# Kernel tuning notes

Measured on AMD Instinct MI355X. Metric: run time of the kernel, lower is better.

Reference implementation:

```python
import jax, jax.numpy as jnp
import numpy as np

H, C = 2, 32  # heads, out_channels per head
NEG_SLOPE = 0.2


def gatv2_layer(h, src, dst, ea, W, b, We, att, bias, N):
    # shared lin_l = lin_r (share_weights=True)
    z = (h @ W + b).reshape(N, H, C)                      # [N,H,C]
    e = (ea @ We).reshape(-1, H, C)                        # [E',H,C]
    s = jax.nn.leaky_relu(z[dst] + z[src] + e, NEG_SLOPE)  # [E',H,C]
    alpha = jnp.einsum('ehc,hc->eh', s, att)               # [E',H]
    # segment softmax over destination neighborhoods
    m = jax.ops.segment_max(alpha, dst, num_segments=N)
    m = jnp.where(jnp.isfinite(m), m, 0.0)
    ex = jnp.exp(alpha - m[dst])
    denom = jax.ops.segment_sum(ex, dst, num_segments=N)
    a = ex / (denom[dst] + 1e-16)                          # [E',H]
    msg = (z[src] * a[:, :, None]).reshape(-1, H * C)      # [E',H*C]
    out = jax.ops.segment_sum(msg, dst, num_segments=N) + bias
    return out                                             # [N,H*C]


def setup_inputs() -> dict:
    key = jax.random.key(0)
    ks = jax.random.split(key, 16)
    N, E = 50000, 800000
    inp = {
        'x': jax.random.normal(ks[0], (N, 2), jnp.float32),
        'edge_index': jax.random.randint(ks[1], (2, E), 0, N, jnp.int64 if jax.config.jax_enable_x64 else jnp.int32).astype(jnp.int32),
        'edge_attr': jax.random.uniform(ks[2], (E, 2), jnp.float32),
        'dest_index': 123,
        'W0': jax.random.normal(ks[3], (2, 64), jnp.float32) * 0.5,
        'b0': jnp.zeros((64,), jnp.float32),
        'We0': jax.random.normal(ks[4], (2, 64), jnp.float32) * 0.5,
        'att0': jax.random.normal(ks[5], (H, C), jnp.float32) * 0.5,
        'bias0': jnp.zeros((64,), jnp.float32),
        'W1': jax.random.normal(ks[6], (64, 64), jnp.float32) * 0.125,
        'b1': jnp.zeros((64,), jnp.float32),
        'We1': jax.random.normal(ks[7], (2, 64), jnp.float32) * 0.5,
        'att1': jax.random.normal(ks[8], (H, C), jnp.float32) * 0.5,
        'bias1': jnp.zeros((64,), jnp.float32),
        'Wm1': jax.random.normal(ks[9], (194, 32), jnp.float32) * 0.07,
        'bm1': jnp.zeros((32,), jnp.float32),
        'Wm2': jax.random.normal(ks[10], (32, 1), jnp.float32) * 0.17,
        'bm2': jnp.zeros((1,), jnp.float32),
    }
    return inp


def reference(x, edge_index, edge_attr, dest_index,
              W0, b0, We0, att0, bias0,
              W1, b1, We1, att1, bias1,
              Wm1, bm1, Wm2, bm2):
    N = x.shape[0]
    # add self loops (fill_value='mean' for edge_attr)
    loops = jnp.arange(N, dtype=edge_index.dtype)
    src = jnp.concatenate([edge_index[0], loops])
    dst = jnp.concatenate([edge_index[1], loops])
    ea_sl = jnp.concatenate(
        [edge_attr, jnp.broadcast_to(edge_attr.mean(axis=0), (N, edge_attr.shape[1]))], axis=0)

    h = x
    h = jax.nn.elu(gatv2_layer(h, src, dst, ea_sl, W0, b0, We0, att0, bias0, N))
    h = jax.nn.elu(gatv2_layer(h, src, dst, ea_sl, W1, b1, We1, att1, bias1, N))

    goal = h[dest_index]                                   # [64]
    src_emb = h[edge_index[0]]                             # [E,64]
    dst_emb = h[edge_index[1]]                             # [E,64]
    goal_rep = jnp.broadcast_to(goal, (edge_index.shape[1], goal.shape[0]))
    edge_in = jnp.concatenate([src_emb, dst_emb, goal_rep, edge_attr], axis=-1)  # [E,194]
    hmlp = jax.nn.relu(edge_in @ Wm1 + bm1)
    logits = (hmlp @ Wm2 + bm2).squeeze(-1)                # [E]
    return logits
```

## Files before the change

### kernel.cpp

```cpp
#include <hip/hip_runtime.h>
#include <hip/hip_bf16.h>
#include <math.h>


typedef __attribute__((ext_vector_type(8))) short short8;
typedef __attribute__((ext_vector_type(4))) float f32x4;

#define BSH 7
#define CH 4096

template <int IMM>
__device__ __forceinline__ float swz(float x) {
    return __int_as_float(__builtin_amdgcn_ds_swizzle(__float_as_int(x), IMM));
}

template <int CTRL>
__device__ __forceinline__ float dpp_add(float p) {
    int t = __builtin_amdgcn_update_dpp(0, __float_as_int(p), CTRL, 0xF, 0xF, true);
    return p + __int_as_float(t);
}

__device__ __forceinline__ float head_reduce(float p) {
    p = dpp_add<0xB1>(p);
    p = dpp_add<0x4E>(p);
    p = dpp_add<0x141>(p);
    p = dpp_add<0x140>(p);
    p += swz<0x401F>(p);
    return p;
}

__device__ __forceinline__ short2 bsplit(float x) {
    unsigned u = __float_as_uint(x);
    short hi = (short)(u >> 16);
    float hif = __uint_as_float(u & 0xFFFF0000u);
    short lo = (short)(__float_as_uint(x - hif) >> 16);
    return make_short2(hi, lo);
}

__global__ void init_kernel(int* __restrict__ bucket_base, float* __restrict__ easum,
                            int nbuck) {
    int i = blockIdx.x * blockDim.x + threadIdx.x;
    if (i < nbuck) bucket_base[i] = 0;
    if (i < 2) easum[i] = 0.f;
}

__global__ __launch_bounds__(256) void easum_kernel(const float2* __restrict__ ea,
                                                    float* __restrict__ easum, int E) {
    __shared__ float r0[4], r1[4];
    int stride = gridDim.x * blockDim.x;
    float s0 = 0.f, s1 = 0.f;
    for (int e = blockIdx.x * blockDim.x + threadIdx.x; e < E; e += stride) {
        float2 v = ea[e];
        s0 += v.x; s1 += v.y;
    }
#pragma unroll
    for (int o = 32; o >= 1; o >>= 1) {
        s0 += __shfl_xor(s0, o);
        s1 += __shfl_xor(s1, o);
    }
    int wave = threadIdx.x >> 6;
    if ((threadIdx.x & 63) == 0) { r0[wave] = s0; r1[wave] = s1; }
    __syncthreads();
    if (threadIdx.x == 0) {
        atomicAdd(&easum[0], r0[0] + r0[1] + r0[2] + r0[3]);
        atomicAdd(&easum[1], r1[0] + r1[1] + r1[2] + r1[3]);
    }
}

__global__ __launch_bounds__(256) void bhist_kernel(const int* __restrict__ ei,
                                                    int* __restrict__ bucket_base,
                                                    int E, int EP, int nbuck) {
    extern __shared__ int lcnt[];
    int tid = threadIdx.x;
    for (int i = tid; i < nbuck; i += 256) lcnt[i] = 0;
    __syncthreads();
    int base = blockIdx.x * CH;
    int end = min(base + CH, EP);
    for (int i = base + tid; i < end; i += 256) {
        int d = (i < E) ? ei[E + i] : (i - E);
        atomicAdd(&lcnt[d >> BSH], 1);
    }
    __syncthreads();
    for (int i = tid; i < nbuck; i += 256) {
        int c = lcnt[i];
        if (c) atomicAdd(&bucket_base[i], c);
    }
}

__global__ __launch_bounds__(256) void bscan_kernel(int* __restrict__ bucket_base,
                                                    int* __restrict__ bucket_cursor,
                                                    int* __restrict__ row_ptr,
                                                    int N, int nbuck) {
    __shared__ int sm[256];
    int tid = threadIdx.x;
    int K = (nbuck + 255) / 256;
    int b0 = tid * K;
    int local = 0;
    for (int k = 0; k < K; ++k) {
        int b = b0 + k;
        if (b < nbuck) local += bucket_base[b];
    }
    sm[tid] = local;
    __syncthreads();
    for (int st = 1; st < 256; st <<= 1) {
        int v = sm[tid];
        int a = (tid >= st) ? sm[tid - st] : 0;
        __syncthreads();
        sm[tid] = v + a;
        __syncthreads();
    }
    int run = (tid == 0) ? 0 : sm[tid - 1];
    for (int k = 0; k < K; ++k) {
        int b = b0 + k;
        if (b < nbuck) {
            int c = bucket_base[b];
            bucket_base[b] = run;
            bucket_cursor[b] = run;
            run += c;
        }
    }
    if (tid == 255) {
        bucket_base[nbuck] = sm[255];
        row_ptr[N] = sm[255];
    }
}

__global__ __launch_bounds__(256) void phaseA_kernel(const int* __restrict__ ei,
                                                     const float2* __restrict__ ea,
                                                     const float* __restrict__ easum,
                                                     int* __restrict__ bucket_cursor,
                                                     float4* __restrict__ staged,
                                                     int E, int EP, int nbuck) {
    extern __shared__ int sm[];
    int* lcnt = sm;
    int* lbase = sm + nbuck;
    int tid = threadIdx.x;
    for (int i = tid; i < nbuck; i += 256) lcnt[i] = 0;
    __syncthreads();
    int base = blockIdx.x * CH;
    int end = min(base + CH, EP);
    for (int i = base + tid; i < end; i += 256) {
        int d = (i < E) ? ei[E + i] : (i - E);
        atomicAdd(&lcnt[d >> BSH], 1);
    }
    __syncthreads();
    for (int i = tid; i < nbuck; i += 256) {
        int c = lcnt[i];
        lbase[i] = c ? atomicAdd(&bucket_cursor[i], c) : 0;
        lcnt[i] = 0;
    }
    __syncthreads();
    float inv = 1.f / (float)E;
    float m0 = easum[0] * inv, m1 = easum[1] * inv;
    for (int i = base + tid; i < end; i += 256) {
        int s, d; float ex, ey;
        if (i < E) {
            s = ei[i]; d = ei[E + i];
            float2 v = ea[i]; ex = v.x; ey = v.y;
        } else {
            s = d = i - E; ex = m0; ey = m1;
        }
        int b = d >> BSH;
        int pos = lbase[b] + atomicAdd(&lcnt[b], 1);
        staged[pos] = make_float4(__int_as_float(s), ex, ey, __int_as_float(d));
    }
}

__global__ __launch_bounds__(256) void phaseB_kernel(const float4* __restrict__ staged,
                                                     const int* __restrict__ bucket_base,
                                                     int* __restrict__ row_ptr,
                                                     float4* __restrict__ recs, int N) {
    __shared__ int cnt128[128];
    __shared__ int offs[128];
    int b = blockIdx.x;
    int n0 = b << BSH;
    int tid = threadIdx.x;
    if (tid < 128) cnt128[tid] = 0;
    __syncthreads();
    int begs = bucket_base[b];
    int ends = bucket_base[b + 1];
    for (int i = begs + tid; i < ends; i += 256) {
        int d = __float_as_int(staged[i].w);
        atomicAdd(&cnt128[d - n0], 1);
    }
    __syncthreads();
    if (tid < 128) offs[tid] = cnt128[tid];
    __syncthreads();
    for (int st = 1; st < 128; st <<= 1) {
        int v = 0;
        if (tid < 128) {
            v = offs[tid];
            if (tid >= st) v += offs[tid - st];
        }
        __syncthreads();
        if (tid < 128) offs[tid] = v;
        __syncthreads();
    }
    if (tid < 128) {
        int excl = begs + offs[tid] - cnt128[tid];
        int node = n0 + tid;
        if (node < N) row_ptr[node] = excl;
        offs[tid] = excl;
    }
    __syncthreads();
    for (int i = begs + tid; i < ends; i += 256) {
        float4 r = staged[i];
        int d = __float_as_int(r.w);
        int pos = atomicAdd(&offs[d - n0], 1);
        recs[pos] = r;
    }
}

__global__ __launch_bounds__(512) void bfrag_kernel(const float* __restrict__ W1,
                                                    const float* __restrict__ Wm1,
                                                    short* __restrict__ BfW1,
                                                    short* __restrict__ BfWm) {
    int snt = threadIdx.x >> 6;
    int lane = threadIdx.x & 63;
    int s = snt >> 2, nt = snt & 3;
    int col = nt * 16 + (lane & 15);
    short* Bf = blockIdx.x == 0 ? BfW1 : BfWm;
#pragma unroll
    for (int j = 0; j < 8; ++j) {
        int k = s * 32 + (lane >> 4) * 8 + j;
        float v;
        if (blockIdx.x == 0) {
            v = W1[k * 64 + col];
        } else {
            v = (col < 32) ? Wm1[k * 32 + col] : Wm1[(64 + k) * 32 + (col - 32)];
        }
        short2 t = bsplit(v);
        Bf[(snt * 2 + 0) * 512 + lane * 8 + j] = t.x;
        Bf[(snt * 2 + 1) * 512 + lane * 8 + j] = t.y;
    }
}

__global__ __launch_bounds__(256) void mfma_gemm64(const float* __restrict__ h,
                                                   const short* __restrict__ Bf,
                                                   const float* __restrict__ bias,
                                                   float* __restrict__ out, int N) {
    int wave = threadIdx.x >> 6;
    int lane = threadIdx.x & 63;
    int n0 = blockIdx.x * 64 + wave * 16;
    if (n0 >= N) return;
    int m = lane & 15, quad = lane >> 4;
    int arow = n0 + m;
    if (arow > N - 1) arow = N - 1;

    f32x4 acc[4] = {{0.f, 0.f, 0.f, 0.f}, {0.f, 0.f, 0.f, 0.f},
                    {0.f, 0.f, 0.f, 0.f}, {0.f, 0.f, 0.f, 0.f}};
#pragma unroll
    for (int s = 0; s < 2; ++s) {
        const float* ap = h + (size_t)arow * 64 + s * 32 + quad * 8;
        float4 a0 = *(const float4*)ap;
        float4 a1 = *(const float4*)(ap + 4);
        short8 ahi, alo;
        short2 t;
        t = bsplit(a0.x); ahi[0] = t.x; alo[0] = t.y;
        t = bsplit(a0.y); ahi[1] = t.x; alo[1] = t.y;
        t = bsplit(a0.z); ahi[2] = t.x; alo[2] = t.y;
        t = bsplit(a0.w); ahi[3] = t.x; alo[3] = t.y;
        t = bsplit(a1.x); ahi[4] = t.x; alo[4] = t.y;
        t = bsplit(a1.y); ahi[5] = t.x; alo[5] = t.y;
        t = bsplit(a1.z); ahi[6] = t.x; alo[6] = t.y;
        t = bsplit(a1.w); ahi[7] = t.x; alo[7] = t.y;
#pragma unroll
        for (int nt = 0; nt < 4; ++nt) {
            const short* bp = Bf + ((s * 4 + nt) * 2) * 512 + lane * 8;
            short8 bhi = *(const short8*)bp;
            short8 blo = *(const short8*)(bp + 512);
            acc[nt] = __builtin_amdgcn_mfma_f32_16x16x32_bf16(ahi, bhi, acc[nt], 0, 0, 0);
            acc[nt] = __builtin_amdgcn_mfma_f32_16x16x32_bf16(ahi, blo, acc[nt], 0, 0, 0);
            acc[nt] = __builtin_amdgcn_mfma_f32_16x16x32_bf16(alo, bhi, acc[nt], 0, 0, 0);
        }
    }
#pragma unroll
    for (int nt = 0; nt < 4; ++nt) {
        int col = nt * 16 + m;
        float bj = bias ? bias[col] : 0.f;
#pragma unroll
        for (int r = 0; r < 4; ++r) {
            int orow = n0 + quad * 4 + r;
            if (orow < N) out[(size_t)orow * 64 + col] = acc[nt][r] + bj;
        }
    }
}

__global__ __launch_bounds__(256) void agg0_kernel(
    const float2* __restrict__ x, const float* __restrict__ W0,
    const float* __restrict__ b0, const int* __restrict__ row_ptr,
    const float4* __restrict__ recs,
    const float* __restrict__ We, const float* __restrict__ att,
    const float* __restrict__ bias, float* __restrict__ hout, int N) {
    int gtid = blockIdx.x * blockDim.x + threadIdx.x;
    int n = gtid >> 6;
    if (n >= N) return;
    n = __builtin_amdgcn_readfirstlane(n);
    int lane = threadIdx.x & 63;

    float W0a = W0[lane], W0b = W0[64 + lane], b0c = b0[lane];
    float We0 = We[lane], We1 = We[64 + lane];
    float attj = att[lane];
    float2 xn = x[n];
    float zn = fmaf(xn.x, W0a, fmaf(xn.y, W0b, b0c));

    int beg = row_ptr[n], end = row_ptr[n + 1];
    float ll[4] = {0.f, 0.f, 0.f, 0.f};
    float aa[4] = {0.f, 0.f, 0.f, 0.f};
    int i = beg;
    for (; i + 7 < end; i += 8) {
        float w[8], zsv[8];
#pragma unroll
        for (int k = 0; k < 8; ++k) {
            float4 r = recs[i + k];
            int s = __builtin_amdgcn_readfirstlane(__float_as_int(r.x));
            float2 xs = x[s];
            float zs = fmaf(xs.x, W0a, fmaf(xs.y, W0b, b0c));
            float sj = zn + zs + fmaf(r.y, We0, r.z * We1);
            sj = fmaxf(sj, 0.2f * sj);
            float alpha = head_reduce(sj * attj);
            w[k] = __expf(fminf(alpha, 60.f));
            zsv[k] = zs;
        }
#pragma unroll
        for (int k = 0; k < 8; ++k) {
            ll[k & 3] += w[k];
            aa[k & 3] = fmaf(w[k], zsv[k], aa[k & 3]);
        }
    }
    for (; i < end; ++i) {
        float4 r = recs[i];
        int s = __builtin_amdgcn_readfirstlane(__float_as_int(r.x));
        float2 xs = x[s];
        float zs = fmaf(xs.x, W0a, fmaf(xs.y, W0b, b0c));
        float sj = zn + zs + fmaf(r.y, We0, r.z * We1);
        sj = fmaxf(sj, 0.2f * sj);
        float alpha = head_reduce(sj * attj);
        float w = __expf(fminf(alpha, 60.f));
        ll[0] += w;
        aa[0] = fmaf(w, zs, aa[0]);
    }
    float l = (ll[0] + ll[1]) + (ll[2] + ll[3]);
    float acc = (aa[0] + aa[1]) + (aa[2] + aa[3]);
    float v = acc / (l + 1e-16f) + bias[lane];
    v = (v > 0.f) ? v : expm1f(v);
    hout[n * 64 + lane] = v;
}

__global__ __launch_bounds__(256) void agg1_kernel(
    const float* __restrict__ z, const int* __restrict__ row_ptr,
    const float4* __restrict__ recs,
    const float* __restrict__ We, const float* __restrict__ att,
    const float* __restrict__ bias, float* __restrict__ hout, int N) {
    int gtid = blockIdx.x * blockDim.x + threadIdx.x;
    int n = gtid >> 6;
    if (n >= N) return;
    n = __builtin_amdgcn_readfirstlane(n);
    int lane = threadIdx.x & 63;

    float We0 = We[lane], We1 = We[64 + lane];
    float attj = att[lane];
    float zn = z[n * 64 + lane];

    int beg = row_ptr[n], end = row_ptr[n + 1];
    float ll[4] = {0.f, 0.f, 0.f, 0.f};
    float aa[4] = {0.f, 0.f, 0.f, 0.f};
    int i = beg;
    for (; i + 7 < end; i += 8) {
        float w[8], zsv[8];
#pragma unroll
        for (int k = 0; k < 8; ++k) {
            float4 r = recs[i + k];
            int s = __builtin_amdgcn_readfirstlane(__float_as_int(r.x));
            float zs = z[s * 64 + lane];
            float sj = zn + zs + fmaf(r.y, We0, r.z * We1);
            sj = fmaxf(sj, 0.2f * sj);
            float alpha = head_reduce(sj * attj);
            w[k] = __expf(fminf(alpha, 60.f));
            zsv[k] = zs;
        }
#pragma unroll
        for (int k = 0; k < 8; ++k) {
            ll[k & 3] += w[k];
            aa[k & 3] = fmaf(w[k], zsv[k], aa[k & 3]);
        }
    }
    for (; i < end; ++i) {
        float4 r = recs[i];
        int s = __builtin_amdgcn_readfirstlane(__float_as_int(r.x));
        float zs = z[s * 64 + lane];
        float sj = zn + zs + fmaf(r.y, We0, r.z * We1);
        sj = fmaxf(sj, 0.2f * sj);
        float alpha = head_reduce(sj * attj);
        float w = __expf(fminf(alpha, 60.f));
        ll[0] += w;
        aa[0] = fmaf(w, zs, aa[0]);
    }
    float l = (ll[0] + ll[1]) + (ll[2] + ll[3]);
    float acc = (aa[0] + aa[1]) + (aa[2] + aa[3]);
    float v = acc / (l + 1e-16f) + bias[lane];
    v = (v > 0.f) ? v : expm1f(v);
    hout[n * 64 + lane] = v;
}

__global__ void gvec_kernel(const float* __restrict__ h, const float* __restrict__ Wm1,
                            const float* __restrict__ bm1, const int* __restrict__ dest,
                            float* __restrict__ gvec) {
    int q = threadIdx.x;
    if (q >= 32) return;
    int d = dest[0];
    float acc = bm1[q];
    for (int k = 0; k < 64; ++k)
        acc = fmaf(h[d * 64 + k], Wm1[(128 + k) * 32 + q], acc);
    gvec[q] = acc;
}

__global__ __launch_bounds__(256) void edge_mlp_kernel(
    const int* __restrict__ ei, const float2* __restrict__ ea,
    const float* __restrict__ hsd, const float* __restrict__ gvec,
    const float* __restrict__ WrowA, const float* __restrict__ WrowB,
    const float* __restrict__ Wm2, const float* __restrict__ bm2,
    float* __restrict__ out, int E) {
    int tid = blockIdx.x * blockDim.x + threadIdx.x;
    int e = tid >> 3;
    int j = tid & 7;
    if (e >= E) return;
    int s = ei[e], d = ei[E + e];
    float2 eav = ea[e];
    float4 a = *(const float4*)(hsd + (size_t)s * 64 + j * 4);
    float4 bv = *(const float4*)(hsd + (size_t)d * 64 + 32 + j * 4);
    float4 g = *(const float4*)(gvec + j * 4);
    float4 wa = *(const float4*)(WrowA + j * 4);
    float4 wb = *(const float4*)(WrowB + j * 4);
    float4 w2 = *(const float4*)(Wm2 + j * 4);
    float acc = 0.f, v;
    v = fmaf(eav.x, wa.x, fmaf(eav.y, wb.x, a.x + bv.x + g.x)); v = fmaxf(v, 0.f); acc = fmaf(v, w2.x, acc);
    v = fmaf(eav.x, wa.y, fmaf(eav.y, wb.y, a.y + bv.y + g.y)); v = fmaxf(v, 0.f); acc = fmaf(v, w2.y, acc);
    v = fmaf(eav.x, wa.z, fmaf(eav.y, wb.z, a.z + bv.z + g.z)); v = fmaxf(v, 0.f); acc = fmaf(v, w2.z, acc);
    v = fmaf(eav.x, wa.w, fmaf(eav.y, wb.w, a.w + bv.w + g.w)); v = fmaxf(v, 0.f); acc = fmaf(v, w2.w, acc);
    acc = dpp_add<0xB1>(acc);
    acc = dpp_add<0x4E>(acc);
    acc = dpp_add<0x141>(acc);
    if (j == 0) out[e] = acc + bm2[0];
}

extern "C" void kernel_launch(void* const* d_in, const int* in_sizes, int n_in,
                              void* d_out, int out_size, void* d_ws, size_t ws_size,
                              hipStream_t stream) {
    const float* x     = (const float*)d_in[0];
    const int*   ei    = (const int*)d_in[1];
    const float* ea    = (const float*)d_in[2];
    const int*   dest  = (const int*)d_in[3];
    const float* W0    = (const float*)d_in[4];
    const float* b0    = (const float*)d_in[5];
    const float* We0   = (const float*)d_in[6];
    const float* att0  = (const float*)d_in[7];
    const float* bias0 = (const float*)d_in[8];
    const float* W1    = (const float*)d_in[9];
    const float* b1    = (const float*)d_in[10];
    const float* We1   = (const float*)d_in[11];
    const float* att1  = (const float*)d_in[12];
    const float* bias1 = (const float*)d_in[13];
    const float* Wm1   = (const float*)d_in[14];
    const float* bm1   = (const float*)d_in[15];
    const float* Wm2   = (const float*)d_in[16];
    const float* bm2   = (const float*)d_in[17];

    const int N = in_sizes[0] / 2;
    const int E = in_sizes[1] / 2;
    const int EP = E + N;
    const int nbuck = (N + 127) >> BSH;
    const int nchunk = (EP + CH - 1) / CH;

    char* ws = (char*)d_ws;
    size_t off = 0;
    auto alloc = [&](size_t bytes) -> void* {
        void* p = ws + off;
        off += bytes;
        off = (off + 255) & ~(size_t)255;
        return p;
    };
    int*    bucket_base   = (int*)alloc((size_t)(nbuck + 1) * 4);
    int*    bucket_cursor = (int*)alloc((size_t)nbuck * 4);
    int*    row_ptr       = (int*)alloc((size_t)(N + 1) * 4);
    size_t  shared_bytes  = (size_t)EP * 16 > (size_t)N * 256 ? (size_t)EP * 16
                                                              : (size_t)N * 256;
    float4* staged        = (float4*)alloc(shared_bytes);
    float4* recs          = (float4*)alloc((size_t)EP * 16);
    float*  hbuf          = (float*)alloc((size_t)N * 64 * 4);
    float*  easum         = (float*)alloc(8);
    float*  gvec          = (float*)alloc(32 * 4);
    short*  BfW1          = (short*)alloc(8192 * 2);
    short*  BfWm          = (short*)alloc(8192 * 2);
    float*  zbuf          = (float*)staged;
    float*  hsd           = zbuf;

    dim3 blk(256);
    init_kernel<<<(nbuck + 255) / 256, blk, 0, stream>>>(bucket_base, easum, nbuck);
    easum_kernel<<<128, blk, 0, stream>>>((const float2*)ea, easum, E);
    bhist_kernel<<<nchunk, blk, (size_t)nbuck * 4, stream>>>(ei, bucket_base, E, EP, nbuck);
    bscan_kernel<<<1, blk, 0, stream>>>(bucket_base, bucket_cursor, row_ptr, N, nbuck);
    phaseA_kernel<<<nchunk, blk, (size_t)nbuck * 8, stream>>>(ei, (const float2*)ea, easum,
                                                              bucket_cursor, staged, E, EP, nbuck);
    phaseB_kernel<<<nbuck, blk, 0, stream>>>(staged, bucket_base, row_ptr, recs, N);
    bfrag_kernel<<<2, 512, 0, stream>>>(W1, Wm1, BfW1, BfWm);
    agg0_kernel<<<(N * 64 + 255) / 256, blk, 0, stream>>>((const float2*)x, W0, b0,
                                                          row_ptr, recs,
                                                          We0, att0, bias0, hbuf, N);
    mfma_gemm64<<<(N + 63) / 64, blk, 0, stream>>>(hbuf, BfW1, b1, zbuf, N);
    agg1_kernel<<<(N * 64 + 255) / 256, blk, 0, stream>>>(zbuf, row_ptr, recs,
                                                          We1, att1, bias1, hbuf, N);
    gvec_kernel<<<1, 64, 0, stream>>>(hbuf, Wm1, bm1, dest, gvec);
    mfma_gemm64<<<(N + 63) / 64, blk, 0, stream>>>(hbuf, BfWm, (const float*)nullptr, hsd, N);
    edge_mlp_kernel<<<((size_t)E * 8 + 255) / 256, blk, 0, stream>>>(
        ei, (const float2*)ea, hsd, gvec,
        Wm1 + 192 * 32, Wm1 + 193 * 32, Wm2, bm2, (float*)d_out, E);
}
```

Measured before the change: 293.0 us.

## Fuse setup kernels and batch attention head reductions across eight edges

Merges the init, easum, histogram, bfrag and gvec launches into fewer kernels (setup_kernel, pre_kernel, and gvec folded into the second GEMM), which removes several tiny launches. In both aggregation kernels the per-edge full head reduction is replaced by a partial DPP reduction per edge. Eight edges' partials are then interleaved across lanes so a single final reduce and a single exp serve all eight, and the results are broadcast back with swizzles. The scalar tail loop is removed by clamping record indices and masking weights. This cuts cross-lane and transcendental work per edge, at the cost of extra selects and some wasted work on padded tail iterations.

```diff
diff --git a/kernel.cpp b/kernel.cpp
--- a/kernel.cpp
+++ b/kernel.cpp
@@ -18,15 +18,6 @@
 __device__ __forceinline__ float dpp_add(float p) {
     int t = __builtin_amdgcn_update_dpp(0, __float_as_int(p), CTRL, 0xF, 0xF, true);
     return p + __int_as_float(t);
-}
-
-__device__ __forceinline__ float head_reduce(float p) {
-    p = dpp_add<0xB1>(p);
-    p = dpp_add<0x4E>(p);
-    p = dpp_add<0x141>(p);
-    p = dpp_add<0x140>(p);
-    p += swz<0x401F>(p);
-    return p;
 }
 
 __device__ __forceinline__ short2 bsplit(float x) {
@@ -37,19 +28,49 @@
     return make_short2(hi, lo);
 }
 
-__global__ void init_kernel(int* __restrict__ bucket_base, float* __restrict__ easum,
-                            int nbuck) {
-    int i = blockIdx.x * blockDim.x + threadIdx.x;
-    if (i < nbuck) bucket_base[i] = 0;
-    if (i < 2) easum[i] = 0.f;
-}
-
-__global__ __launch_bounds__(256) void easum_kernel(const float2* __restrict__ ea,
-                                                    float* __restrict__ easum, int E) {
+__global__ __launch_bounds__(512) void setup_kernel(const float* __restrict__ W1,
+                                                    const float* __restrict__ Wm1,
+                                                    short* __restrict__ BfW1,
+                                                    short* __restrict__ BfWm,
+                                                    int* __restrict__ bucket_base,
+                                                    float* __restrict__ easum, int nbuck) {
+    if (blockIdx.x == 2) {
+        for (int i = threadIdx.x; i <= nbuck; i += 512) bucket_base[i] = 0;
+        if (threadIdx.x < 2) easum[threadIdx.x] = 0.f;
+        return;
+    }
+    int snt = threadIdx.x >> 6;
+    int lane = threadIdx.x & 63;
+    int s = snt >> 2, nt = snt & 3;
+    int col = nt * 16 + (lane & 15);
+    short* Bf = blockIdx.x == 0 ? BfW1 : BfWm;
+#pragma unroll
+    for (int j = 0; j < 8; ++j) {
+        int k = s * 32 + (lane >> 4) * 8 + j;
+        float v;
+        if (blockIdx.x == 0) {
+            v = W1[k * 64 + col];
+        } else {
+            v = (col < 32) ? Wm1[k * 32 + col] : Wm1[(64 + k) * 32 + (col - 32)];
+        }
+        short2 t = bsplit(v);
+        Bf[(snt * 2 + 0) * 512 + lane * 8 + j] = t.x;
+        Bf[(snt * 2 + 1) * 512 + lane * 8 + j] = t.y;
+    }
+}
+
+__global__ __launch_bounds__(256) void pre_kernel(const int* __restrict__ ei,
+                                                  const float2* __restrict__ ea,
+                                                  int* __restrict__ bucket_base,
+                                                  float* __restrict__ easum,
+                                                  int E, int EP, int nbuck) {
+    extern __shared__ int lcnt[];
     __shared__ float r0[4], r1[4];
-    int stride = gridDim.x * blockDim.x;
+    int tid = threadIdx.x;
+    for (int i = tid; i < nbuck; i += 256) lcnt[i] = 0;
     float s0 = 0.f, s1 = 0.f;
-    for (int e = blockIdx.x * blockDim.x + threadIdx.x; e < E; e += stride) {
+    int estride = gridDim.x * 256;
+    for (int e = blockIdx.x * 256 + tid; e < E; e += estride) {
         float2 v = ea[e];
         s0 += v.x; s1 += v.y;
     }
@@ -58,21 +79,8 @@
         s0 += __shfl_xor(s0, o);
         s1 += __shfl_xor(s1, o);
     }
-    int wave = threadIdx.x >> 6;
-    if ((threadIdx.x & 63) == 0) { r0[wave] = s0; r1[wave] = s1; }
-    __syncthreads();
-    if (threadIdx.x == 0) {
-        atomicAdd(&easum[0], r0[0] + r0[1] + r0[2] + r0[3]);
-        atomicAdd(&easum[1], r1[0] + r1[1] + r1[2] + r1[3]);
-    }
-}
-
-__global__ __launch_bounds__(256) void bhist_kernel(const int* __restrict__ ei,
-                                                    int* __restrict__ bucket_base,
-                                                    int E, int EP, int nbuck) {
-    extern __shared__ int lcnt[];
-    int tid = threadIdx.x;
-    for (int i = tid; i < nbuck; i += 256) lcnt[i] = 0;
+    int wave = tid >> 6;
+    if ((tid & 63) == 0) { r0[wave] = s0; r1[wave] = s1; }
     __syncthreads();
     int base = blockIdx.x * CH;
     int end = min(base + CH, EP);
@@ -81,6 +89,10 @@
         atomicAdd(&lcnt[d >> BSH], 1);
     }
     __syncthreads();
+    if (tid == 0) {
+        atomicAdd(&easum[0], r0[0] + r0[1] + r0[2] + r0[3]);
+        atomicAdd(&easum[1], r1[0] + r1[1] + r1[2] + r1[3]);
+    }
     for (int i = tid; i < nbuck; i += 256) {
         int c = lcnt[i];
         if (c) atomicAdd(&bucket_base[i], c);
@@ -211,81 +223,6 @@
     }
 }
 
-__global__ __launch_bounds__(512) void bfrag_kernel(const float* __restrict__ W1,
-                                                    const float* __restrict__ Wm1,
-                                                    short* __restrict__ BfW1,
-                                                    short* __restrict__ BfWm) {
-    int snt = threadIdx.x >> 6;
-    int lane = threadIdx.x & 63;
-    int s = snt >> 2, nt = snt & 3;
-    int col = nt * 16 + (lane & 15);
-    short* Bf = blockIdx.x == 0 ? BfW1 : BfWm;
-#pragma unroll
-    for (int j = 0; j < 8; ++j) {
-        int k = s * 32 + (lane >> 4) * 8 + j;
-        float v;
-        if (blockIdx.x == 0) {
-            v = W1[k * 64 + col];
-        } else {
-            v = (col < 32) ? Wm1[k * 32 + col] : Wm1[(64 + k) * 32 + (col - 32)];
-        }
-        short2 t = bsplit(v);
-        Bf[(snt * 2 + 0) * 512 + lane * 8 + j] = t.x;
-        Bf[(snt * 2 + 1) * 512 + lane * 8 + j] = t.y;
-    }
-}
-
-__global__ __launch_bounds__(256) void mfma_gemm64(const float* __restrict__ h,
-                                                   const short* __restrict__ Bf,
-                                                   const float* __restrict__ bias,
-                                                   float* __restrict__ out, int N) {
-    int wave = threadIdx.x >> 6;
-    int lane = threadIdx.x & 63;
-    int n0 = blockIdx.x * 64 + wave * 16;
-    if (n0 >= N) return;
-    int m = lane & 15, quad = lane >> 4;
-    int arow = n0 + m;
-    if (arow > N - 1) arow = N - 1;
-
-    f32x4 acc[4] = {{0.f, 0.f, 0.f, 0.f}, {0.f, 0.f, 0.f, 0.f},
-                    {0.f, 0.f, 0.f, 0.f}, {0.f, 0.f, 0.f, 0.f}};
-#pragma unroll
-    for (int s = 0; s < 2; ++s) {
-        const float* ap = h + (size_t)arow * 64 + s * 32 + quad * 8;
-        float4 a0 = *(const float4*)ap;
-        float4 a1 = *(const float4*)(ap + 4);
-        short8 ahi, alo;
-        short2 t;
-        t = bsplit(a0.x); ahi[0] = t.x; alo[0] = t.y;
-        t = bsplit(a0.y); ahi[1] = t.x; alo[1] = t.y;
-        t = bsplit(a0.z); ahi[2] = t.x; alo[2] = t.y;
-        t = bsplit(a0.w); ahi[3] = t.x; alo[3] = t.y;
-        t = bsplit(a1.x); ahi[4] = t.x; alo[4] = t.y;
-        t = bsplit(a1.y); ahi[5] = t.x; alo[5] = t.y;
-        t = bsplit(a1.z); ahi[6] = t.x; alo[6] = t.y;
-        t = bsplit(a1.w); ahi[7] = t.x; alo[7] = t.y;
-#pragma unroll
-        for (int nt = 0; nt < 4; ++nt) {
-            const short* bp = Bf + ((s * 4 + nt) * 2) * 512 + lane * 8;
-            short8 bhi = *(const short8*)bp;
-            short8 blo = *(const short8*)(bp + 512);
-            acc[nt] = __builtin_amdgcn_mfma_f32_16x16x32_bf16(ahi, bhi, acc[nt], 0, 0, 0);
-            acc[nt] = __builtin_amdgcn_mfma_f32_16x16x32_bf16(ahi, blo, acc[nt], 0, 0, 0);
-            acc[nt] = __builtin_amdgcn_mfma_f32_16x16x32_bf16(alo, bhi, acc[nt], 0, 0, 0);
-        }
-    }
-#pragma unroll
-    for (int nt = 0; nt < 4; ++nt) {
-        int col = nt * 16 + m;
-        float bj = bias ? bias[col] : 0.f;
-#pragma unroll
-        for (int r = 0; r < 4; ++r) {
-            int orow = n0 + quad * 4 + r;
-            if (orow < N) out[(size_t)orow * 64 + col] = acc[nt][r] + bj;
-        }
-    }
-}
-
 __global__ __launch_bounds__(256) void agg0_kernel(
     const float2* __restrict__ x, const float* __restrict__ W0,
     const float* __restrict__ b0, const int* __restrict__ row_ptr,
@@ -297,6 +234,7 @@
     if (n >= N) return;
     n = __builtin_amdgcn_readfirstlane(n);
     int lane = threadIdx.x & 63;
+    bool c0 = lane & 1, c1 = lane & 2, c2 = lane & 4;
 
     float W0a = W0[lane], W0b = W0[64 + lane], b0c = b0[lane];
     float We0 = We[lane], We1 = We[64 + lane];
@@ -307,44 +245,54 @@
     int beg = row_ptr[n], end = row_ptr[n + 1];
     float ll[4] = {0.f, 0.f, 0.f, 0.f};
     float aa[4] = {0.f, 0.f, 0.f, 0.f};
-    int i = beg;
-    for (; i + 7 < end; i += 8) {
-        float w[8], zsv[8];
+    for (int i = beg; i < end; i += 8) {
+        float p[8], zs[8], ry[8], rz[8];
 #pragma unroll
         for (int k = 0; k < 8; ++k) {
-            float4 r = recs[i + k];
+            int idx = i + k; if (idx > end - 1) idx = end - 1;
+            float4 r = recs[idx];
             int s = __builtin_amdgcn_readfirstlane(__float_as_int(r.x));
             float2 xs = x[s];
-            float zs = fmaf(xs.x, W0a, fmaf(xs.y, W0b, b0c));
-            float sj = zn + zs + fmaf(r.y, We0, r.z * We1);
+            zs[k] = fmaf(xs.x, W0a, fmaf(xs.y, W0b, b0c));
+            ry[k] = r.y; rz[k] = r.z;
+        }
+#pragma unroll
+        for (int k = 0; k < 8; ++k) {
+            float sj = zn + zs[k] + fmaf(ry[k], We0, rz[k] * We1);
             sj = fmaxf(sj, 0.2f * sj);
-            float alpha = head_reduce(sj * attj);
-            w[k] = __expf(fminf(alpha, 60.f));
-            zsv[k] = zs;
-        }
+            float t = sj * attj;
+            t = dpp_add<0xB1>(t);
+            t = dpp_add<0x4E>(t);
+            t = dpp_add<0x141>(t);
+            p[k] = t;
+        }
+        float t0 = c0 ? p[1] : p[0];
+        float t1 = c0 ? p[3] : p[2];
+        float t2 = c0 ? p[5] : p[4];
+        float t3 = c0 ? p[7] : p[6];
+        float u0 = c1 ? t1 : t0;
+        float u1 = c1 ? t3 : t2;
+        float v  = c2 ? u1 : u0;
+        v = dpp_add<0x128>(v);
+        v += swz<0x401F>(v);
+        float wall = __expf(fminf(v, 60.f));
+        float wk[8];
+        wk[0] = swz<0x018>(wall); wk[1] = swz<0x038>(wall);
+        wk[2] = swz<0x058>(wall); wk[3] = swz<0x078>(wall);
+        wk[4] = swz<0x098>(wall); wk[5] = swz<0x0B8>(wall);
+        wk[6] = swz<0x0D8>(wall); wk[7] = swz<0x0F8>(wall);
 #pragma unroll
         for (int k = 0; k < 8; ++k) {
-            ll[k & 3] += w[k];
-            aa[k & 3] = fmaf(w[k], zsv[k], aa[k & 3]);
-        }
-    }
-    for (; i < end; ++i) {
-        float4 r = recs[i];
-        int s = __builtin_amdgcn_readfirstlane(__float_as_int(r.x));
-        float2 xs = x[s];
-        float zs = fmaf(xs.x, W0a, fmaf(xs.y, W0b, b0c));
-        float sj = zn + zs + fmaf(r.y, We0, r.z * We1);
-        sj = fmaxf(sj, 0.2f * sj);
-        float alpha = head_reduce(sj * attj);
-        float w = __expf(fminf(alpha, 60.f));
-        ll[0] += w;
-        aa[0] = fmaf(w, zs, aa[0]);
+            float w = (i + k < end) ? wk[k] : 0.f;
+            ll[k & 3] += w;
+            aa[k & 3] = fmaf(w, zs[k], aa[k & 3]);
+        }
     }
     float l = (ll[0] + ll[1]) + (ll[2] + ll[3]);
-    float acc = (aa[0] + aa[1]) + (aa[2] + aa[3]);
-    float v = acc / (l + 1e-16f) + bias[lane];
+    float a = (aa[0] + aa[1]) + (aa[2] + aa[3]);
+    float v = a / (l + 1e-16f) + bias[lane];
     v = (v > 0.f) ? v : expm1f(v);
-    hout[n * 64 + lane] = v;
+    hout[(size_t)n * 64 + lane] = v;
 }
 
 __global__ __launch_bounds__(256) void agg1_kernel(
@@ -357,62 +305,127 @@
     if (n >= N) return;
     n = __builtin_amdgcn_readfirstlane(n);
     int lane = threadIdx.x & 63;
+    bool c0 = lane & 1, c1 = lane & 2, c2 = lane & 4;
 
     float We0 = We[lane], We1 = We[64 + lane];
     float attj = att[lane];
-    float zn = z[n * 64 + lane];
+    float zn = z[(size_t)n * 64 + lane];
 
     int beg = row_ptr[n], end = row_ptr[n + 1];
     float ll[4] = {0.f, 0.f, 0.f, 0.f};
     float aa[4] = {0.f, 0.f, 0.f, 0.f};
-    int i = beg;
-    for (; i + 7 < end; i += 8) {
-        float w[8], zsv[8];
+    for (int i = beg; i < end; i += 8) {
+        float p[8], zs[8], ry[8], rz[8];
+        int sidx[8];
 #pragma unroll
         for (int k = 0; k < 8; ++k) {
-            float4 r = recs[i + k];
-            int s = __builtin_amdgcn_readfirstlane(__float_as_int(r.x));
-            float zs = z[s * 64 + lane];
-            float sj = zn + zs + fmaf(r.y, We0, r.z * We1);
+            int idx = i + k; if (idx > end - 1) idx = end - 1;
+            float4 r = recs[idx];
+            sidx[k] = __builtin_amdgcn_readfirstlane(__float_as_int(r.x));
+            ry[k] = r.y; rz[k] = r.z;
+        }
+#pragma unroll
+        for (int k = 0; k < 8; ++k) zs[k] = z[(size_t)sidx[k] * 64 + lane];
+#pragma unroll
+        for (int k = 0; k < 8; ++k) {
+            float sj = zn + zs[k] + fmaf(ry[k], We0, rz[k] * We1);
             sj = fmaxf(sj, 0.2f * sj);
-            float alpha = head_reduce(sj * attj);
-            w[k] = __expf(fminf(alpha, 60.f));
-            zsv[k] = zs;
-        }
+            float t = sj * attj;
+            t = dpp_add<0xB1>(t);
+            t = dpp_add<0x4E>(t);
+            t = dpp_add<0x141>(t);
+            p[k] = t;
+        }
+        float t0 = c0 ? p[1] : p[0];
+        float t1 = c0 ? p[3] : p[2];
+        float t2 = c0 ? p[5] : p[4];
+        float t3 = c0 ? p[7] : p[6];
+        float u0 = c1 ? t1 : t0;
+        float u1 = c1 ? t3 : t2;
+        float v  = c2 ? u1 : u0;
+        v = dpp_add<0x128>(v);
+        v += swz<0x401F>(v);
+        float wall = __expf(fminf(v, 60.f));
+        float wk[8];
+        wk[0] = swz<0x018>(wall); wk[1] = swz<0x038>(wall);
+        wk[2] = swz<0x058>(wall); wk[3] = swz<0x078>(wall);
+        wk[4] = swz<0x098>(wall); wk[5] = swz<0x0B8>(wall);
+        wk[6] = swz<0x0D8>(wall); wk[7] = swz<0x0F8>(wall);
 #pragma unroll
         for (int k = 0; k < 8; ++k) {
-            ll[k & 3] += w[k];
-            aa[k & 3] = fmaf(w[k], zsv[k], aa[k & 3]);
-        }
-    }
-    for (; i < end; ++i) {
-        float4 r = recs[i];
-        int s = __builtin_amdgcn_readfirstlane(__float_as_int(r.x));
-        float zs = z[s * 64 + lane];
-        float sj = zn + zs + fmaf(r.y, We0, r.z * We1);
-        sj = fmaxf(sj, 0.2f * sj);
-        float alpha = head_reduce(sj * attj);
-        float w = __expf(fminf(alpha, 60.f));
-        ll[0] += w;
-        aa[0] = fmaf(w, zs, aa[0]);
+            float w = (i + k < end) ? wk[k] : 0.f;
+            ll[k & 3] += w;
+            aa[k & 3] = fmaf(w, zs[k], aa[k & 3]);
+        }
     }
     float l = (ll[0] + ll[1]) + (ll[2] + ll[3]);
-    float acc = (aa[0] + aa[1]) + (aa[2] + aa[3]);
-    float v = acc / (l + 1e-16f) + bias[lane];
+    float a = (aa[0] + aa[1]) + (aa[2] + aa[3]);
+    float v = a / (l + 1e-16f) + bias[lane];
     v = (v > 0.f) ? v : expm1f(v);
-    hout[n * 64 + lane] = v;
-}
-
-__global__ void gvec_kernel(const float* __restrict__ h, const float* __restrict__ Wm1,
-                            const float* __restrict__ bm1, const int* __restrict__ dest,
-                            float* __restrict__ gvec) {
-    int q = threadIdx.x;
-    if (q >= 32) return;
-    int d = dest[0];
-    float acc = bm1[q];
-    for (int k = 0; k < 64; ++k)
-        acc = fmaf(h[d * 64 + k], Wm1[(128 + k) * 32 + q], acc);
-    gvec[q] = acc;
+    hout[(size_t)n * 64 + lane] = v;
+}
+
+__global__ __launch_bounds__(256) void mfma_gemm64(const float* __restrict__ h,
+                                                   const short* __restrict__ Bf,
+                                                   const float* __restrict__ bias,
+                                                   float* __restrict__ out, int N,
+                                                   const float* __restrict__ Wm1,
+                                                   const float* __restrict__ bm1,
+                                                   const int* __restrict__ dest,
+                                                   float* __restrict__ gv) {
+    int wave = threadIdx.x >> 6;
+    int lane = threadIdx.x & 63;
+    int n0 = blockIdx.x * 64 + wave * 16;
+    if (n0 < N) {
+        int m = lane & 15, quad = lane >> 4;
+        int arow = n0 + m;
+        if (arow > N - 1) arow = N - 1;
+        f32x4 acc[4] = {{0.f, 0.f, 0.f, 0.f}, {0.f, 0.f, 0.f, 0.f},
+                        {0.f, 0.f, 0.f, 0.f}, {0.f, 0.f, 0.f, 0.f}};
+#pragma unroll
+        for (int s = 0; s < 2; ++s) {
+            const float* ap = h + (size_t)arow * 64 + s * 32 + quad * 8;
+            float4 a0 = *(const float4*)ap;
+            float4 a1 = *(const float4*)(ap + 4);
+            short8 ahi, alo;
+            short2 t;
+            t = bsplit(a0.x); ahi[0] = t.x; alo[0] = t.y;
+            t = bsplit(a0.y); ahi[1] = t.x; alo[1] = t.y;
+            t = bsplit(a0.z); ahi[2] = t.x; alo[2] = t.y;
+            t = bsplit(a0.w); ahi[3] = t.x; alo[3] = t.y;
+            t = bsplit(a1.x); ahi[4] = t.x; alo[4] = t.y;
+            t = bsplit(a1.y); ahi[5] = t.x; alo[5] = t.y;
+            t = bsplit(a1.z); ahi[6] = t.x; alo[6] = t.y;
+            t = bsplit(a1.w); ahi[7] = t.x; alo[7] = t.y;
+#pragma unroll
+            for (int nt = 0; nt < 4; ++nt) {
+                const short* bp = Bf + ((s * 4 + nt) * 2) * 512 + lane * 8;
+                short8 bhi = *(const short8*)bp;
+                short8 blo = *(const short8*)(bp + 512);
+                acc[nt] = __builtin_amdgcn_mfma_f32_16x16x32_bf16(ahi, bhi, acc[nt], 0, 0, 0);
+                acc[nt] = __builtin_amdgcn_mfma_f32_16x16x32_bf16(ahi, blo, acc[nt], 0, 0, 0);
+                acc[nt] = __builtin_amdgcn_mfma_f32_16x16x32_bf16(alo, bhi, acc[nt], 0, 0, 0);
+            }
+        }
+#pragma unroll
+        for (int nt = 0; nt < 4; ++nt) {
+            int col = nt * 16 + m;
+            float bj = bias ? bias[col] : 0.f;
+#pragma unroll
+            for (int r = 0; r < 4; ++r) {
+                int orow = n0 + quad * 4 + r;
+                if (orow < N) out[(size_t)orow * 64 + col] = acc[nt][r] + bj;
+            }
+        }
+    }
+    if (gv && blockIdx.x == 0 && threadIdx.x < 32) {
+        int dd = dest[0];
+        int q = threadIdx.x;
+        float acc2 = bm1[q];
+        for (int k = 0; k < 64; ++k)
+            acc2 = fmaf(h[(size_t)dd * 64 + k], Wm1[(128 + k) * 32 + q], acc2);
+        gv[q] = acc2;
+    }
 }
 
 __global__ __launch_bounds__(256) void edge_mlp_kernel(
@@ -496,22 +509,22 @@
     float*  hsd           = zbuf;
 
     dim3 blk(256);
-    init_kernel<<<(nbuck + 255) / 256, blk, 0, stream>>>(bucket_base, easum, nbuck);
-    easum_kernel<<<128, blk, 0, stream>>>((const float2*)ea, easum, E);
-    bhist_kernel<<<nchunk, blk, (size_t)nbuck * 4, stream>>>(ei, bucket_base, E, EP, nbuck);
+    setup_kernel<<<3, 512, 0, stream>>>(W1, Wm1, BfW1, BfWm, bucket_base, easum, nbuck);
+    pre_kernel<<<nchunk, blk, (size_t)nbuck * 4, stream>>>(ei, (const float2*)ea,
+                                                           bucket_base, easum, E, EP, nbuck);
     bscan_kernel<<<1, blk, 0, stream>>>(bucket_base, bucket_cursor, row_ptr, N, nbuck);
     phaseA_kernel<<<nchunk, blk, (size_t)nbuck * 8, stream>>>(ei, (const float2*)ea, easum,
                                                               bucket_cursor, staged, E, EP, nbuck);
     phaseB_kernel<<<nbuck, blk, 0, stream>>>(staged, bucket_base, row_ptr, recs, N);
-    bfrag_kernel<<<2, 512, 0, stream>>>(W1, Wm1, BfW1, BfWm);
     agg0_kernel<<<(N * 64 + 255) / 256, blk, 0, stream>>>((const float2*)x, W0, b0,
                                                           row_ptr, recs,
                                                           We0, att0, bias0, hbuf, N);
-    mfma_gemm64<<<(N + 63) / 64, blk, 0, stream>>>(hbuf, BfW1, b1, zbuf, N);
+    mfma_gemm64<<<(N + 63) / 64, blk, 0, stream>>>(hbuf, BfW1, b1, zbuf, N,
+                                                   nullptr, nullptr, nullptr, nullptr);
     agg1_kernel<<<(N * 64 + 255) / 256, blk, 0, stream>>>(zbuf, row_ptr, recs,
                                                           We1, att1, bias1, hbuf, N);
-    gvec_kernel<<<1, 64, 0, stream>>>(hbuf, Wm1, bm1, dest, gvec);
-    mfma_gemm64<<<(N + 63) / 64, blk, 0, stream>>>(hbuf, BfWm, (const float*)nullptr, hsd, N);
+    mfma_gemm64<<<(N + 63) / 64, blk, 0, stream>>>(hbuf, BfWm, (const float*)nullptr, hsd, N,
+                                                   Wm1, bm1, dest, gvec);
     edge_mlp_kernel<<<((size_t)E * 8 + 255) / 256, blk, 0, stream>>>(
         ei, (const float2*)ea, hsd, gvec,
         Wm1 + 192 * 32, Wm1 + 193 * 32, Wm2, bm2, (float*)d_out, E);
```

Result: faster. 285.1 us (-2.7%).
